# Optimization experiments

Measured on AMD Instinct MI355X. Metric: run time of the kernel, lower is better.

The kernel has to match this reference:

```python
import jax, jax.numpy as jnp
import numpy as np

B, S, D, H = 2, 2048, 2048, 16
DH = D // H            # attention_inner_dim = 128
FF = 4 * D             # feedforward_inner_dim = 8192
EPS = 1e-6


def layernorm(x, gamma, beta):
    m = jnp.mean(x, axis=-1, keepdims=True)
    v = jnp.mean((x - m) ** 2, axis=-1, keepdims=True)
    return gamma * (x - m) / jnp.sqrt(v + EPS) + beta


def rotate_half(x):
    # source rotate_half: swap halves without negation
    h = x.shape[-1] // 2
    return jnp.concatenate([x[..., h:], x[..., :h]], axis=-1)


def setup_inputs() -> dict:
    key = jax.random.key(0)
    ks = jax.random.split(key, 8)
    d = {}
    d['x'] = jax.random.normal(ks[0], (B, S, D), dtype=jnp.float32) * 0.02
    d['W_fused'] = jax.random.normal(ks[1], (D, 3 * D + FF), dtype=jnp.float32) * (D ** -0.5)
    d['b_fused'] = jnp.zeros((3 * D + FF,), dtype=jnp.float32)
    d['W_attn'] = jax.random.normal(ks[2], (D, D), dtype=jnp.float32) * (D ** -0.5)
    d['b_attn'] = jnp.zeros((D,), dtype=jnp.float32)
    d['W_ff'] = jax.random.normal(ks[3], (FF, D), dtype=jnp.float32) * (FF ** -0.5)
    d['b_ff'] = jnp.zeros((D,), dtype=jnp.float32)
    d['gamma1'] = jnp.ones((FF,), dtype=jnp.float32)
    d['beta1'] = jnp.zeros((FF,), dtype=jnp.float32)
    d['gamma2'] = jnp.ones((D,), dtype=jnp.float32)
    d['beta2'] = jnp.zeros((D,), dtype=jnp.float32)
    # learned rotary table, shape [n_positions>=S, head_dim], std = head_dim**-0.5
    d['rope_w'] = jax.random.normal(ks[4], (S, DH), dtype=jnp.float32) * (DH ** -0.5)
    return d


def reference(x, W_fused, b_fused, W_attn, b_attn, W_ff, b_ff,
              gamma1, beta1, gamma2, beta2, rope_w):
    # fused QKV + FFN projection (single GEMM)
    fused = x @ W_fused + b_fused                       # [B,S,3D+FF]
    q, k, v, ff = jnp.split(fused, [D, 2 * D, 3 * D], axis=-1)
    q = q.reshape(B, S, H, DH).transpose(0, 2, 1, 3)    # [B,H,S,DH]
    k = k.reshape(B, S, H, DH).transpose(0, 2, 1, 3)
    v = v.reshape(B, S, H, DH).transpose(0, 2, 1, 3)

    # inline rotary embedding from learned per-position table
    pe = rope_w[:S]                                     # [S,DH]
    cos, sin = jnp.cos(pe), jnp.sin(pe)

    def rope(t):
        return t * cos + rotate_half(t) * sin

    q = rope(q) * (DH ** -0.5)
    k = rope(k)

    # manual causal attention
    sim = jnp.einsum('bhqd,bhkd->bhqk', q, k)           # [B,H,S,S]
    causal = jnp.tril(jnp.ones((S, S), dtype=bool))
    sim = jnp.where(causal, sim, jnp.finfo(sim.dtype).min)
    attn_w = jax.nn.softmax(sim, axis=-1)
    o = jnp.einsum('bhqk,bhkd->bhqd', attn_w, v)        # [B,H,S,DH]
    o = o.transpose(0, 2, 1, 3).reshape(B, S, D)
    attn = o @ W_attn + b_attn                          # [B,S,D]

    # parallel feedforward branch: norm -> relu -> proj -> silu (SwiGLU in src is x*sigmoid(x))
    h = jax.nn.relu(layernorm(ff, gamma1, beta1))
    ffo = h @ W_ff + b_ff
    ffo = ffo * jax.nn.sigmoid(ffo)

    return layernorm(attn + ffo, gamma2, beta2)
```

## Files before the change

### kernel.cpp

```cpp
#include <hip/hip_runtime.h>
#include <hip/hip_bf16.h>
#include <cmath>

#define BB 2
#define SS 2048
#define DD 2048
#define HHN 16
#define DHH 128
#define FFF 8192
#define NFF (3*DD+FFF)
#define MR (BB*SS)
#define LNEPS 1e-6f

typedef __hip_bfloat16 bf16;
using bf16x8 = __attribute__((ext_vector_type(8))) __bf16;
using f32x4  = __attribute__((ext_vector_type(4))) float;

__device__ __forceinline__ void async_copy16(const bf16* g, bf16* l) {
  __builtin_amdgcn_global_load_lds(
      (const __attribute__((address_space(1))) void*)g,
      (__attribute__((address_space(3))) void*)l, 16, 0, 0);
}

__global__ __launch_bounds__(256) void k_convert(const float* __restrict__ in,
                                                 bf16* __restrict__ out, int n4) {
  int i = blockIdx.x * 256 + threadIdx.x;
  if (i >= n4) return;
  float4 v = ((const float4*)in)[i];
  out[4*i+0] = __float2bfloat16(v.x);
  out[4*i+1] = __float2bfloat16(v.y);
  out[4*i+2] = __float2bfloat16(v.z);
  out[4*i+3] = __float2bfloat16(v.w);
}

__global__ __launch_bounds__(256) void k_transpose(const float* __restrict__ in,
                                                   bf16* __restrict__ out, int R, int C) {
  __shared__ float tile[32][33];
  int c0 = blockIdx.x * 32, r0 = blockIdx.y * 32;
  int tx = threadIdx.x, ty = threadIdx.y;
  #pragma unroll
  for (int i = 0; i < 32; i += 8)
    tile[ty + i][tx] = in[(size_t)(r0 + ty + i) * C + (c0 + tx)];
  __syncthreads();
  #pragma unroll
  for (int i = 0; i < 32; i += 8)
    out[(size_t)(c0 + ty + i) * R + (r0 + tx)] = __float2bfloat16(tile[tx][ty + i]);
}

__global__ void k_vtrans(const bf16* __restrict__ fused, bf16* __restrict__ vT) {
  __shared__ bf16 tile[32][33];
  int s0 = blockIdx.x * 32, d0 = blockIdx.y * 32, bh = blockIdx.z;
  int b = bh >> 4, h = bh & 15;
  int tx = threadIdx.x, ty = threadIdx.y;
  const bf16* src = fused + (size_t)(b * SS) * NFF + 2 * DD + h * DHH;
  #pragma unroll
  for (int i = 0; i < 32; i += 8)
    tile[ty + i][tx] = src[(size_t)(s0 + ty + i) * NFF + d0 + tx];
  __syncthreads();
  bf16* dst = vT + ((size_t)bh * DHH) * SS;
  #pragma unroll
  for (int i = 0; i < 32; i += 8)
    dst[(size_t)(d0 + ty + i) * SS + s0 + tx] = tile[tx][ty + i];
}

__global__ __launch_bounds__(256) void k_gemm_bt(const bf16* __restrict__ A,
                                                 const bf16* __restrict__ BT,
                                                 const float* __restrict__ bias,
                                                 void* __restrict__ Cout,
                                                 const float* __restrict__ addin,
                                                 int M, int N, int K, int mode) {
  __shared__ __align__(16) bf16 As[128 * 32];
  __shared__ __align__(16) bf16 Bs[128 * 32];
  int NBm = M >> 7;
  constexpr int PW = 16;
  int bid = blockIdx.x;
  int pid = bid / (PW * NBm), rem = bid % (PW * NBm);
  int by = rem / PW, bx = pid * PW + rem % PW;
  int tid = threadIdx.x;
  int w = tid >> 6, l = tid & 63;
  int wm = w >> 1, wn = w & 1;
  int l15 = l & 15, g = l >> 4;
  int sr4 = l >> 2, sc4 = (l & 3) * 8;
  int m0 = by * 128, n0 = bx * 128;

  f32x4 acc[4][4];
  #pragma unroll
  for (int i = 0; i < 4; i++)
    #pragma unroll
    for (int j = 0; j < 4; j++)
      acc[i][j] = f32x4{0.f, 0.f, 0.f, 0.f};

  for (int k0 = 0; k0 < K; k0 += 32) {
    __syncthreads();
    #pragma unroll
    for (int i = 0; i < 2; i++) {
      int r = (w * 2 + i) * 16 + sr4;
      async_copy16(A + (size_t)(m0 + r) * K + k0 + sc4, &As[r * 32 + sc4]);
      async_copy16(BT + (size_t)(n0 + r) * K + k0 + sc4, &Bs[r * 32 + sc4]);
    }
    __syncthreads();

    bf16x8 af[4], bf_[4];
    #pragma unroll
    for (int i = 0; i < 4; i++)
      af[i] = *reinterpret_cast<const bf16x8*>(&As[(wm * 64 + i * 16 + l15) * 32 + g * 8]);
    #pragma unroll
    for (int j = 0; j < 4; j++)
      bf_[j] = *reinterpret_cast<const bf16x8*>(&Bs[(wn * 64 + j * 16 + l15) * 32 + g * 8]);
    #pragma unroll
    for (int i = 0; i < 4; i++)
      #pragma unroll
      for (int j = 0; j < 4; j++)
        acc[i][j] = __builtin_amdgcn_mfma_f32_16x16x32_bf16(af[i], bf_[j], acc[i][j], 0, 0, 0);
  }

  float* Cf = (float*)Cout;
  bf16* Cb = (bf16*)Cout;
  #pragma unroll
  for (int i = 0; i < 4; i++) {
    #pragma unroll
    for (int j = 0; j < 4; j++) {
      int mbase = m0 + wm * 64 + i * 16 + g * 4;
      int nn = n0 + wn * 64 + j * 16 + l15;
      float bv = bias[nn];
      #pragma unroll
      for (int rr = 0; rr < 4; rr++) {
        size_t idx = (size_t)(mbase + rr) * N + nn;
        float v = acc[i][j][rr] + bv;
        if (mode == 0) {
          Cf[idx] = v;
        } else if (mode == 1) {
          Cb[idx] = __float2bfloat16(v);
        } else {
          float sig = 1.f / (1.f + expf(-v));
          Cf[idx] = addin[idx] + v * sig;
        }
      }
    }
  }
}

__global__ __launch_bounds__(256) void k_sincos(const float* __restrict__ rope_w,
                                                float2* __restrict__ tab) {
  int i = blockIdx.x * 256 + threadIdx.x;
  if (i >= SS * DHH) return;
  float v = rope_w[i];
  tab[i] = make_float2(cosf(v), sinf(v));
}

__global__ __launch_bounds__(256) void k_rope(bf16* __restrict__ fused,
                                              const float2* __restrict__ tab) {
  int row = blockIdx.x;
  int s = row & (SS - 1);
  const float2* tr = tab + (size_t)s * DHH;
  int tid = threadIdx.x;
  int isK = tid >> 7, ch = tid & 127;
  int h = ch >> 3, c0 = (ch & 7) * 8;
  const float scale = 0.08838834764831845f;
  bf16* base = fused + (size_t)row * NFF + isK * DD + h * DHH;
  bf16x8 lo = *reinterpret_cast<const bf16x8*>(base + c0);
  bf16x8 hi = *reinterpret_cast<const bf16x8*>(base + c0 + 64);
  bf16x8 olo, ohi;
  #pragma unroll
  for (int t = 0; t < 8; t++) {
    int d = c0 + t;
    float2 cl = tr[d], chh = tr[d + 64];
    float x0 = (float)lo[t], x1 = (float)hi[t];
    float r0 = x0 * cl.x + x1 * cl.y;
    float r1 = x1 * chh.x + x0 * chh.y;
    if (!isK) { r0 *= scale; r1 *= scale; }
    olo[t] = (__bf16)r0;
    ohi[t] = (__bf16)r1;
  }
  *reinterpret_cast<bf16x8*>(base + c0) = olo;
  *reinterpret_cast<bf16x8*>(base + c0 + 64) = ohi;
}

__global__ __launch_bounds__(256) void k_flash(const bf16* __restrict__ fused,
                                               const bf16* __restrict__ vT,
                                               bf16* __restrict__ obuf) {
  __shared__ __align__(16) bf16 smem[20480];
  bf16* Ks = smem;
  bf16* Vt = smem + 8192;
  bf16* Ps = smem + 16384;
  bf16* Qs = smem;

  int qb = blockIdx.x, bh = blockIdx.y;
  int b = bh >> 4, h = bh & 15;
  int tid = threadIdx.x;
  int w = tid >> 6, l = tid & 63;
  int l15 = l & 15, g = l >> 4;

  const bf16* qbase = fused + (size_t)(b * SS + qb * 64) * NFF + h * DHH;
  const bf16* kbase = fused + (size_t)(b * SS) * NFF + DD + h * DHH;
  const bf16* vtb = vT + (size_t)bh * DHH * SS;

  #pragma unroll
  for (int ks = 0; ks < 4; ks++)
    async_copy16(qbase + (size_t)(w * 16 + (l >> 2)) * NFF + ks * 32 + (l & 3) * 8,
                 &Qs[ks * 2048 + w * 512 + l * 8]);
  __syncthreads();
  bf16x8 qf[4];
  #pragma unroll
  for (int ks = 0; ks < 4; ks++)
    qf[ks] = *reinterpret_cast<const bf16x8*>(&Qs[ks * 2048 + (w * 16 + l15) * 32 + g * 8]);

  f32x4 o[8];
  #pragma unroll
  for (int nt = 0; nt < 8; nt++) o[nt] = f32x4{0.f, 0.f, 0.f, 0.f};
  float m_i[4], l_i[4];
  #pragma unroll
  for (int r = 0; r < 4; r++) { m_i[r] = -1e30f; l_i[r] = 0.f; }
  int qrow_base = qb * 64 + w * 16 + g * 4;

  for (int kt = 0; kt <= qb; kt++) {
    __syncthreads();
    #pragma unroll
    for (int ks = 0; ks < 4; ks++)
      async_copy16(kbase + (size_t)(kt * 64 + w * 16 + (l >> 2)) * NFF + ks * 32 + (l & 3) * 8,
                   &Ks[ks * 2048 + w * 512 + l * 8]);
    #pragma unroll
    for (int j = 0; j < 2; j++)
      #pragma unroll
      for (int kc = 0; kc < 2; kc++)
        async_copy16(vtb + (size_t)(j * 64 + w * 16 + (l >> 2)) * SS + kt * 64 + kc * 32 + (l & 3) * 8,
                     &Vt[kc * 4096 + j * 2048 + w * 512 + l * 8]);
    __syncthreads();

    f32x4 s[4];
    #pragma unroll
    for (int nt = 0; nt < 4; nt++) {
      s[nt] = f32x4{0.f, 0.f, 0.f, 0.f};
      #pragma unroll
      for (int ks = 0; ks < 4; ks++) {
        bf16x8 bfrag = *reinterpret_cast<const bf16x8*>(
            &Ks[ks * 2048 + (nt * 16 + l15) * 32 + g * 8]);
        s[nt] = __builtin_amdgcn_mfma_f32_16x16x32_bf16(qf[ks], bfrag, s[nt], 0, 0, 0);
      }
    }
    #pragma unroll
    for (int nt = 0; nt < 4; nt++) {
      int kk = kt * 64 + nt * 16 + l15;
      #pragma unroll
      for (int r = 0; r < 4; r++)
        if (kk > qrow_base + r) s[nt][r] = -1e30f;
    }
    float alpha[4];
    #pragma unroll
    for (int r = 0; r < 4; r++) {
      float mx = fmaxf(fmaxf(s[0][r], s[1][r]), fmaxf(s[2][r], s[3][r]));
      mx = fmaxf(mx, __shfl_xor(mx, 1));
      mx = fmaxf(mx, __shfl_xor(mx, 2));
      mx = fmaxf(mx, __shfl_xor(mx, 4));
      mx = fmaxf(mx, __shfl_xor(mx, 8));
      float mnew = fmaxf(m_i[r], mx);
      alpha[r] = __expf(m_i[r] - mnew);
      m_i[r] = mnew;
      float ls = 0.f;
      #pragma unroll
      for (int nt = 0; nt < 4; nt++) {
        float p = __expf(s[nt][r] - mnew);
        s[nt][r] = p;
        ls += p;
      }
      ls += __shfl_xor(ls, 1);
      ls += __shfl_xor(ls, 2);
      ls += __shfl_xor(ls, 4);
      ls += __shfl_xor(ls, 8);
      l_i[r] = l_i[r] * alpha[r] + ls;
    }
    #pragma unroll
    for (int nt = 0; nt < 4; nt++) {
      int kk = nt * 16 + l15;
      #pragma unroll
      for (int r = 0; r < 4; r++)
        *(__bf16*)&Ps[(kk >> 5) * 2048 + (w * 16 + g * 4 + r) * 32 + (kk & 31)] =
            (__bf16)s[nt][r];
    }
    #pragma unroll
    for (int nt = 0; nt < 8; nt++)
      #pragma unroll
      for (int r = 0; r < 4; r++) o[nt][r] *= alpha[r];
    bf16x8 pf[2];
    #pragma unroll
    for (int ks = 0; ks < 2; ks++)
      pf[ks] = *reinterpret_cast<const bf16x8*>(
          &Ps[ks * 2048 + (w * 16 + l15) * 32 + g * 8]);
    #pragma unroll
    for (int nt = 0; nt < 8; nt++)
      #pragma unroll
      for (int ks = 0; ks < 2; ks++) {
        bf16x8 bfrag = *reinterpret_cast<const bf16x8*>(
            &Vt[ks * 4096 + (nt * 16 + l15) * 32 + g * 8]);
        o[nt] = __builtin_amdgcn_mfma_f32_16x16x32_bf16(pf[ks], bfrag, o[nt], 0, 0, 0);
      }
  }

  float inv[4];
  #pragma unroll
  for (int r = 0; r < 4; r++) inv[r] = 1.f / l_i[r];
  #pragma unroll
  for (int nt = 0; nt < 8; nt++)
    #pragma unroll
    for (int r = 0; r < 4; r++) {
      size_t row = (size_t)(b * SS + qrow_base + r);
      obuf[row * DD + h * DHH + nt * 16 + l15] = __float2bfloat16(o[nt][r] * inv[r]);
    }
}

__global__ __launch_bounds__(256) void k_ln1_relu(const bf16* __restrict__ fused,
                                                  const float* __restrict__ gamma,
                                                  const float* __restrict__ beta,
                                                  bf16* __restrict__ h) {
  int row = blockIdx.x;
  const bf16* xr = fused + (size_t)row * NFF + 3 * DD;
  int tid = threadIdx.x;
  bf16x8 v8[4];
  float s = 0.f, ss = 0.f;
  #pragma unroll
  for (int k = 0; k < 4; k++) {
    v8[k] = *reinterpret_cast<const bf16x8*>(xr + (tid + k * 256) * 8);
    #pragma unroll
    for (int t = 0; t < 8; t++) {
      float v = (float)v8[k][t];
      s += v; ss += v * v;
    }
  }
  #pragma unroll
  for (int off = 32; off > 0; off >>= 1) { s += __shfl_down(s, off); ss += __shfl_down(ss, off); }
  __shared__ float red[8];
  int wave = tid >> 6, lane = tid & 63;
  if (lane == 0) { red[wave] = s; red[4 + wave] = ss; }
  __syncthreads();
  if (tid == 0) {
    float S0 = red[0] + red[1] + red[2] + red[3];
    float SQ = red[4] + red[5] + red[6] + red[7];
    float m = S0 / FFF;
    float var = SQ / FFF - m * m;
    red[0] = m;
    red[1] = 1.f / sqrtf(var + LNEPS);
  }
  __syncthreads();
  float m = red[0], inv = red[1];
  bf16* hr = h + (size_t)row * FFF;
  #pragma unroll
  for (int k = 0; k < 4; k++) {
    bf16x8 o8;
    int base = (tid + k * 256) * 8;
    #pragma unroll
    for (int t = 0; t < 8; t++) {
      float v = (float)v8[k][t];
      float y = gamma[base + t] * (v - m) * inv + beta[base + t];
      o8[t] = (__bf16)fmaxf(y, 0.f);
    }
    *reinterpret_cast<bf16x8*>(hr + base) = o8;
  }
}

__global__ __launch_bounds__(256) void k_ln2(const float* __restrict__ yin,
                                             const float* __restrict__ gamma,
                                             const float* __restrict__ beta,
                                             float* __restrict__ out) {
  int row = blockIdx.x;
  const float4* xr = (const float4*)(yin + (size_t)row * DD);
  int tid = threadIdx.x;
  float4 v4[2];
  float s = 0.f, ss = 0.f;
  #pragma unroll
  for (int k = 0; k < 2; k++) {
    v4[k] = xr[tid + k * 256];
    s += v4[k].x + v4[k].y + v4[k].z + v4[k].w;
    ss += v4[k].x * v4[k].x + v4[k].y * v4[k].y + v4[k].z * v4[k].z + v4[k].w * v4[k].w;
  }
  #pragma unroll
  for (int off = 32; off > 0; off >>= 1) { s += __shfl_down(s, off); ss += __shfl_down(ss, off); }
  __shared__ float red[8];
  int wave = tid >> 6, lane = tid & 63;
  if (lane == 0) { red[wave] = s; red[4 + wave] = ss; }
  __syncthreads();
  if (tid == 0) {
    float S0 = red[0] + red[1] + red[2] + red[3];
    float SQ = red[4] + red[5] + red[6] + red[7];
    float m = S0 / DD;
    float var = SQ / DD - m * m;
    red[0] = m;
    red[1] = 1.f / sqrtf(var + LNEPS);
  }
  __syncthreads();
  float m = red[0], inv = red[1];
  float4* orow = (float4*)(out + (size_t)row * DD);
  #pragma unroll
  for (int k = 0; k < 2; k++) {
    int base = (tid + k * 256) * 4;
    float4 r;
    r.x = gamma[base + 0] * (v4[k].x - m) * inv + beta[base + 0];
    r.y = gamma[base + 1] * (v4[k].y - m) * inv + beta[base + 1];
    r.z = gamma[base + 2] * (v4[k].z - m) * inv + beta[base + 2];
    r.w = gamma[base + 3] * (v4[k].w - m) * inv + beta[base + 3];
    orow[tid + k * 256] = r;
  }
}

extern "C" void kernel_launch(void* const* d_in, const int* in_sizes, int n_in,
                              void* d_out, int out_size, void* d_ws, size_t ws_size,
                              hipStream_t stream) {
  const float* x       = (const float*)d_in[0];
  const float* W_fused = (const float*)d_in[1];
  const float* b_fused = (const float*)d_in[2];
  const float* W_attn  = (const float*)d_in[3];
  const float* b_attn  = (const float*)d_in[4];
  const float* W_ff    = (const float*)d_in[5];
  const float* b_ff    = (const float*)d_in[6];
  const float* gamma1  = (const float*)d_in[7];
  const float* beta1   = (const float*)d_in[8];
  const float* gamma2  = (const float*)d_in[9];
  const float* beta2   = (const float*)d_in[10];
  const float* rope_w  = (const float*)d_in[11];

  char* ws = (char*)d_ws;
  size_t off = 0;
  auto alloc = [&](size_t bytes) -> void* {
    void* p = ws + off;
    off += (bytes + 255) & ~(size_t)255;
    return p;
  };
  bf16* fused = (bf16*)alloc((size_t)MR * NFF * 2);
  bf16* xb    = (bf16*)alloc((size_t)MR * DD * 2);
  bf16* WfT   = (bf16*)alloc((size_t)NFF * DD * 2);
  bf16* WaT   = (bf16*)alloc((size_t)DD * DD * 2);
  bf16* WffT  = (bf16*)alloc((size_t)DD * FFF * 2);
  bf16* hbuf  = (bf16*)alloc((size_t)MR * FFF * 2);
  bf16* obuf  = (bf16*)alloc((size_t)MR * DD * 2);
  float* ybuf = (float*)alloc((size_t)MR * DD * 4);
  if (off > ws_size) return;
  bf16* vT = xb;
  float2* tab = (float2*)ybuf;

  k_convert<<<(MR * DD / 4 + 255) / 256, 256, 0, stream>>>(x, xb, MR * DD / 4);
  k_sincos<<<(SS * DHH + 255) / 256, 256, 0, stream>>>(rope_w, tab);
  k_transpose<<<dim3(NFF / 32, DD / 32), dim3(32, 8), 0, stream>>>(W_fused, WfT, DD, NFF);
  k_transpose<<<dim3(DD / 32, DD / 32), dim3(32, 8), 0, stream>>>(W_attn, WaT, DD, DD);
  k_transpose<<<dim3(DD / 32, FFF / 32), dim3(32, 8), 0, stream>>>(W_ff, WffT, FFF, DD);
  k_gemm_bt<<<(NFF / 128) * (MR / 128), 256, 0, stream>>>(xb, WfT, b_fused, fused, nullptr,
                                                          MR, NFF, DD, 1);
  k_rope<<<MR, 256, 0, stream>>>(fused, tab);
  k_vtrans<<<dim3(SS / 32, DHH / 32, BB * HHN), dim3(32, 8), 0, stream>>>(fused, vT);
  k_flash<<<dim3(SS / 64, BB * HHN), 256, 0, stream>>>(fused, vT, obuf);
  k_gemm_bt<<<(DD / 128) * (MR / 128), 256, 0, stream>>>(obuf, WaT, b_attn, ybuf, nullptr,
                                                         MR, DD, DD, 0);
  k_ln1_relu<<<MR, 256, 0, stream>>>(fused, gamma1, beta1, hbuf);
  k_gemm_bt<<<(DD / 128) * (MR / 128), 256, 0, stream>>>(hbuf, WffT, b_ff, ybuf, ybuf,
                                                         MR, DD, FFF, 2);
  k_ln2<<<MR, 256, 0, stream>>>(ybuf, gamma2, beta2, (float*)d_out);
}
```

Baseline: 1.176 ms.

## Switch GEMM to 32x32x16 MFMA with K=64 tiles and bf16 intermediate output

Rewrites the shared GEMM to use 32x32x16 bf16 MFMA instructions with a 64-wide K step and a k-chunk-major LDS layout, which halves the number of barrier-separated iterations and cuts LDS fragment reads per MFMA. The attention and FFN projection outputs are now stored as bf16 instead of fp32, and the final layernorm reads bf16. This reduces the intermediate buffer's memory traffic at the cost of extra rounding in the residual sum before the final norm. The rope table moves to its own buffer because ybuf is now too small to hold it.

```diff
diff --git a/kernel.cpp b/kernel.cpp
--- a/kernel.cpp
+++ b/kernel.cpp
@@ -15,6 +15,7 @@
 typedef __hip_bfloat16 bf16;
 using bf16x8 = __attribute__((ext_vector_type(8))) __bf16;
 using f32x4  = __attribute__((ext_vector_type(4))) float;
+using f32x16 = __attribute__((ext_vector_type(16))) float;
 
 __device__ __forceinline__ void async_copy16(const bf16* g, bf16* l) {
   __builtin_amdgcn_global_load_lds(
@@ -66,11 +67,11 @@
 __global__ __launch_bounds__(256) void k_gemm_bt(const bf16* __restrict__ A,
                                                  const bf16* __restrict__ BT,
                                                  const float* __restrict__ bias,
-                                                 void* __restrict__ Cout,
-                                                 const float* __restrict__ addin,
+                                                 bf16* __restrict__ Cout,
+                                                 const bf16* __restrict__ addin,
                                                  int M, int N, int K, int mode) {
-  __shared__ __align__(16) bf16 As[128 * 32];
-  __shared__ __align__(16) bf16 Bs[128 * 32];
+  __shared__ __align__(16) bf16 As[8192];
+  __shared__ __align__(16) bf16 Bs[8192];
   int NBm = M >> 7;
   constexpr int PW = 16;
   int bid = blockIdx.x;
@@ -79,62 +80,65 @@
   int tid = threadIdx.x;
   int w = tid >> 6, l = tid & 63;
   int wm = w >> 1, wn = w & 1;
-  int l15 = l & 15, g = l >> 4;
-  int sr4 = l >> 2, sc4 = (l & 3) * 8;
+  int l31 = l & 31, kg = l >> 5;
   int m0 = by * 128, n0 = bx * 128;
 
-  f32x4 acc[4][4];
-  #pragma unroll
-  for (int i = 0; i < 4; i++)
-    #pragma unroll
-    for (int j = 0; j < 4; j++)
-      acc[i][j] = f32x4{0.f, 0.f, 0.f, 0.f};
-
-  for (int k0 = 0; k0 < K; k0 += 32) {
+  f32x16 acc[2][2];
+  #pragma unroll
+  for (int i = 0; i < 2; i++)
+    #pragma unroll
+    for (int j = 0; j < 2; j++)
+      #pragma unroll
+      for (int r = 0; r < 16; r++) acc[i][j][r] = 0.f;
+
+  for (int k0 = 0; k0 < K; k0 += 64) {
     __syncthreads();
     #pragma unroll
-    for (int i = 0; i < 2; i++) {
-      int r = (w * 2 + i) * 16 + sr4;
-      async_copy16(A + (size_t)(m0 + r) * K + k0 + sc4, &As[r * 32 + sc4]);
-      async_copy16(BT + (size_t)(n0 + r) * K + k0 + sc4, &Bs[r * 32 + sc4]);
+    for (int j = 0; j < 4; j++) {
+      int i = j * 4 + w;
+      int c = i >> 1, mm = (i & 1) * 64 + l;
+      async_copy16(A + (size_t)(m0 + mm) * K + k0 + c * 8, &As[(c * 128 + mm) * 8]);
+      async_copy16(BT + (size_t)(n0 + mm) * K + k0 + c * 8, &Bs[(c * 128 + mm) * 8]);
     }
     __syncthreads();
 
-    bf16x8 af[4], bf_[4];
-    #pragma unroll
-    for (int i = 0; i < 4; i++)
-      af[i] = *reinterpret_cast<const bf16x8*>(&As[(wm * 64 + i * 16 + l15) * 32 + g * 8]);
-    #pragma unroll
-    for (int j = 0; j < 4; j++)
-      bf_[j] = *reinterpret_cast<const bf16x8*>(&Bs[(wn * 64 + j * 16 + l15) * 32 + g * 8]);
-    #pragma unroll
-    for (int i = 0; i < 4; i++)
-      #pragma unroll
-      for (int j = 0; j < 4; j++)
-        acc[i][j] = __builtin_amdgcn_mfma_f32_16x16x32_bf16(af[i], bf_[j], acc[i][j], 0, 0, 0);
-  }
-
-  float* Cf = (float*)Cout;
-  bf16* Cb = (bf16*)Cout;
-  #pragma unroll
-  for (int i = 0; i < 4; i++) {
-    #pragma unroll
-    for (int j = 0; j < 4; j++) {
-      int mbase = m0 + wm * 64 + i * 16 + g * 4;
-      int nn = n0 + wn * 64 + j * 16 + l15;
-      float bv = bias[nn];
-      #pragma unroll
-      for (int rr = 0; rr < 4; rr++) {
-        size_t idx = (size_t)(mbase + rr) * N + nn;
-        float v = acc[i][j][rr] + bv;
-        if (mode == 0) {
-          Cf[idx] = v;
-        } else if (mode == 1) {
-          Cb[idx] = __float2bfloat16(v);
-        } else {
+    #pragma unroll
+    for (int t = 0; t < 4; t++) {
+      bf16x8 af[2], bf_[2];
+      #pragma unroll
+      for (int mi = 0; mi < 2; mi++)
+        af[mi] = *reinterpret_cast<const bf16x8*>(
+            &As[((t * 2 + kg) * 128 + wm * 64 + mi * 32 + l31) * 8]);
+      #pragma unroll
+      for (int nj = 0; nj < 2; nj++)
+        bf_[nj] = *reinterpret_cast<const bf16x8*>(
+            &Bs[((t * 2 + kg) * 128 + wn * 64 + nj * 32 + l31) * 8]);
+      #pragma unroll
+      for (int mi = 0; mi < 2; mi++)
+        #pragma unroll
+        for (int nj = 0; nj < 2; nj++)
+          acc[mi][nj] = __builtin_amdgcn_mfma_f32_32x32x16_bf16(
+              af[mi], bf_[nj], acc[mi][nj], 0, 0, 0);
+    }
+  }
+
+  #pragma unroll
+  for (int mi = 0; mi < 2; mi++) {
+    #pragma unroll
+    for (int nj = 0; nj < 2; nj++) {
+      int col = n0 + wn * 64 + nj * 32 + l31;
+      int rbase = m0 + wm * 64 + mi * 32 + 4 * kg;
+      float bv = bias[col];
+      #pragma unroll
+      for (int r = 0; r < 16; r++) {
+        int row = rbase + (r & 3) + 8 * (r >> 2);
+        size_t idx = (size_t)row * N + col;
+        float v = acc[mi][nj][r] + bv;
+        if (mode == 2) {
           float sig = 1.f / (1.f + expf(-v));
-          Cf[idx] = addin[idx] + v * sig;
+          v = __bfloat162float(addin[idx]) + v * sig;
         }
+        Cout[idx] = __float2bfloat16(v);
       }
     }
   }
@@ -357,20 +361,19 @@
   }
 }
 
-__global__ __launch_bounds__(256) void k_ln2(const float* __restrict__ yin,
+__global__ __launch_bounds__(256) void k_ln2(const bf16* __restrict__ yin,
                                              const float* __restrict__ gamma,
                                              const float* __restrict__ beta,
                                              float* __restrict__ out) {
   int row = blockIdx.x;
-  const float4* xr = (const float4*)(yin + (size_t)row * DD);
+  const bf16* xr = yin + (size_t)row * DD;
   int tid = threadIdx.x;
-  float4 v4[2];
+  bf16x8 v8 = *reinterpret_cast<const bf16x8*>(xr + tid * 8);
   float s = 0.f, ss = 0.f;
   #pragma unroll
-  for (int k = 0; k < 2; k++) {
-    v4[k] = xr[tid + k * 256];
-    s += v4[k].x + v4[k].y + v4[k].z + v4[k].w;
-    ss += v4[k].x * v4[k].x + v4[k].y * v4[k].y + v4[k].z * v4[k].z + v4[k].w * v4[k].w;
+  for (int t = 0; t < 8; t++) {
+    float v = (float)v8[t];
+    s += v; ss += v * v;
   }
   #pragma unroll
   for (int off = 32; off > 0; off >>= 1) { s += __shfl_down(s, off); ss += __shfl_down(ss, off); }
@@ -391,13 +394,13 @@
   float4* orow = (float4*)(out + (size_t)row * DD);
   #pragma unroll
   for (int k = 0; k < 2; k++) {
-    int base = (tid + k * 256) * 4;
+    int base = tid * 8 + k * 4;
     float4 r;
-    r.x = gamma[base + 0] * (v4[k].x - m) * inv + beta[base + 0];
-    r.y = gamma[base + 1] * (v4[k].y - m) * inv + beta[base + 1];
-    r.z = gamma[base + 2] * (v4[k].z - m) * inv + beta[base + 2];
-    r.w = gamma[base + 3] * (v4[k].w - m) * inv + beta[base + 3];
-    orow[tid + k * 256] = r;
+    r.x = gamma[base + 0] * ((float)v8[k * 4 + 0] - m) * inv + beta[base + 0];
+    r.y = gamma[base + 1] * ((float)v8[k * 4 + 1] - m) * inv + beta[base + 1];
+    r.z = gamma[base + 2] * ((float)v8[k * 4 + 2] - m) * inv + beta[base + 2];
+    r.w = gamma[base + 3] * ((float)v8[k * 4 + 3] - m) * inv + beta[base + 3];
+    orow[tid * 2 + k] = r;
   }
 }
 
@@ -431,10 +434,11 @@
   bf16* WffT  = (bf16*)alloc((size_t)DD * FFF * 2);
   bf16* hbuf  = (bf16*)alloc((size_t)MR * FFF * 2);
   bf16* obuf  = (bf16*)alloc((size_t)MR * DD * 2);
-  float* ybuf = (float*)alloc((size_t)MR * DD * 4);
+  bf16* ybuf  = (bf16*)alloc((size_t)MR * DD * 2);
+  float* tabf = (float*)alloc((size_t)SS * DHH * 8);
   if (off > ws_size) return;
   bf16* vT = xb;
-  float2* tab = (float2*)ybuf;
+  float2* tab = (float2*)tabf;
 
   k_convert<<<(MR * DD / 4 + 255) / 256, 256, 0, stream>>>(x, xb, MR * DD / 4);
   k_sincos<<<(SS * DHH + 255) / 256, 256, 0, stream>>>(rope_w, tab);
```

Result: slower. 1.511 ms (+28.4%).

## Enlarge flash query tile to 128 rows and store attention/FFN output in bf16

Applied to the files above, without the earlier changes.

The flash attention kernel now gives each block 128 query rows, with each wave handling two 16-row sub-tiles. Every K/V tile loaded into LDS is therefore reused for twice as many queries, which halves K/V global traffic and the number of blocks. Separately, the intermediate attention-plus-FFN sum ybuf is kept in bf16 instead of fp32, which cuts its memory traffic and changes the precision of the final layernorm input. The rope table gets its own workspace buffer, and waves skip fully masked tiles; fewer blocks may reduce occupancy and load balance on the causal triangle.

```diff
diff --git a/kernel.cpp b/kernel.cpp
--- a/kernel.cpp
+++ b/kernel.cpp
@@ -66,8 +66,8 @@
 __global__ __launch_bounds__(256) void k_gemm_bt(const bf16* __restrict__ A,
                                                  const bf16* __restrict__ BT,
                                                  const float* __restrict__ bias,
-                                                 void* __restrict__ Cout,
-                                                 const float* __restrict__ addin,
+                                                 bf16* __restrict__ Cout,
+                                                 const bf16* __restrict__ addin,
                                                  int M, int N, int K, int mode) {
   __shared__ __align__(16) bf16 As[128 * 32];
   __shared__ __align__(16) bf16 Bs[128 * 32];
@@ -114,8 +114,6 @@
         acc[i][j] = __builtin_amdgcn_mfma_f32_16x16x32_bf16(af[i], bf_[j], acc[i][j], 0, 0, 0);
   }
 
-  float* Cf = (float*)Cout;
-  bf16* Cb = (bf16*)Cout;
   #pragma unroll
   for (int i = 0; i < 4; i++) {
     #pragma unroll
@@ -127,14 +125,11 @@
       for (int rr = 0; rr < 4; rr++) {
         size_t idx = (size_t)(mbase + rr) * N + nn;
         float v = acc[i][j][rr] + bv;
-        if (mode == 0) {
-          Cf[idx] = v;
-        } else if (mode == 1) {
-          Cb[idx] = __float2bfloat16(v);
-        } else {
+        if (mode == 2) {
           float sig = 1.f / (1.f + expf(-v));
-          Cf[idx] = addin[idx] + v * sig;
+          v = __bfloat162float(addin[idx]) + v * sig;
         }
+        Cout[idx] = __float2bfloat16(v);
       }
     }
   }
@@ -179,7 +174,7 @@
 __global__ __launch_bounds__(256) void k_flash(const bf16* __restrict__ fused,
                                                const bf16* __restrict__ vT,
                                                bf16* __restrict__ obuf) {
-  __shared__ __align__(16) bf16 smem[20480];
+  __shared__ __align__(16) bf16 smem[24576];
   bf16* Ks = smem;
   bf16* Vt = smem + 8192;
   bf16* Ps = smem + 16384;
@@ -191,29 +186,41 @@
   int w = tid >> 6, l = tid & 63;
   int l15 = l & 15, g = l >> 4;
 
-  const bf16* qbase = fused + (size_t)(b * SS + qb * 64) * NFF + h * DHH;
+  const bf16* qbase = fused + (size_t)(b * SS + qb * 128) * NFF + h * DHH;
   const bf16* kbase = fused + (size_t)(b * SS) * NFF + DD + h * DHH;
   const bf16* vtb = vT + (size_t)bh * DHH * SS;
 
   #pragma unroll
   for (int ks = 0; ks < 4; ks++)
-    async_copy16(qbase + (size_t)(w * 16 + (l >> 2)) * NFF + ks * 32 + (l & 3) * 8,
-                 &Qs[ks * 2048 + w * 512 + l * 8]);
-  __syncthreads();
-  bf16x8 qf[4];
-  #pragma unroll
-  for (int ks = 0; ks < 4; ks++)
-    qf[ks] = *reinterpret_cast<const bf16x8*>(&Qs[ks * 2048 + (w * 16 + l15) * 32 + g * 8]);
-
-  f32x4 o[8];
-  #pragma unroll
-  for (int nt = 0; nt < 8; nt++) o[nt] = f32x4{0.f, 0.f, 0.f, 0.f};
-  float m_i[4], l_i[4];
-  #pragma unroll
-  for (int r = 0; r < 4; r++) { m_i[r] = -1e30f; l_i[r] = 0.f; }
-  int qrow_base = qb * 64 + w * 16 + g * 4;
-
-  for (int kt = 0; kt <= qb; kt++) {
+    #pragma unroll
+    for (int j = 0; j < 2; j++) {
+      int row = w * 32 + j * 16 + (l >> 2);
+      async_copy16(qbase + (size_t)row * NFF + ks * 32 + (l & 3) * 8,
+                   &Qs[ks * 4096 + row * 32 + (l & 3) * 8]);
+    }
+  __syncthreads();
+  bf16x8 qf[2][4];
+  #pragma unroll
+  for (int p = 0; p < 2; p++)
+    #pragma unroll
+    for (int ks = 0; ks < 4; ks++)
+      qf[p][ks] = *reinterpret_cast<const bf16x8*>(
+          &Qs[ks * 4096 + (w * 32 + p * 16 + l15) * 32 + g * 8]);
+
+  f32x4 o[2][8];
+  #pragma unroll
+  for (int p = 0; p < 2; p++)
+    #pragma unroll
+    for (int nt = 0; nt < 8; nt++) o[p][nt] = f32x4{0.f, 0.f, 0.f, 0.f};
+  float m_i[2][4], l_i[2][4];
+  #pragma unroll
+  for (int p = 0; p < 2; p++)
+    #pragma unroll
+    for (int r = 0; r < 4; r++) { m_i[p][r] = -1e30f; l_i[p][r] = 0.f; }
+  int qrow0 = qb * 128 + w * 32 + g * 4;
+
+  int ntiles = 2 * qb + 2;
+  for (int kt = 0; kt < ntiles; kt++) {
     __syncthreads();
     #pragma unroll
     for (int ks = 0; ks < 4; ks++)
@@ -227,85 +234,98 @@
                      &Vt[kc * 4096 + j * 2048 + w * 512 + l * 8]);
     __syncthreads();
 
-    f32x4 s[4];
+    if (kt * 64 > qb * 128 + w * 32 + 31) continue;
+
+    f32x4 s[2][4];
     #pragma unroll
     for (int nt = 0; nt < 4; nt++) {
-      s[nt] = f32x4{0.f, 0.f, 0.f, 0.f};
+      s[0][nt] = f32x4{0.f, 0.f, 0.f, 0.f};
+      s[1][nt] = f32x4{0.f, 0.f, 0.f, 0.f};
       #pragma unroll
       for (int ks = 0; ks < 4; ks++) {
         bf16x8 bfrag = *reinterpret_cast<const bf16x8*>(
             &Ks[ks * 2048 + (nt * 16 + l15) * 32 + g * 8]);
-        s[nt] = __builtin_amdgcn_mfma_f32_16x16x32_bf16(qf[ks], bfrag, s[nt], 0, 0, 0);
-      }
-    }
-    #pragma unroll
-    for (int nt = 0; nt < 4; nt++) {
-      int kk = kt * 64 + nt * 16 + l15;
-      #pragma unroll
-      for (int r = 0; r < 4; r++)
-        if (kk > qrow_base + r) s[nt][r] = -1e30f;
-    }
-    float alpha[4];
-    #pragma unroll
-    for (int r = 0; r < 4; r++) {
-      float mx = fmaxf(fmaxf(s[0][r], s[1][r]), fmaxf(s[2][r], s[3][r]));
-      mx = fmaxf(mx, __shfl_xor(mx, 1));
-      mx = fmaxf(mx, __shfl_xor(mx, 2));
-      mx = fmaxf(mx, __shfl_xor(mx, 4));
-      mx = fmaxf(mx, __shfl_xor(mx, 8));
-      float mnew = fmaxf(m_i[r], mx);
-      alpha[r] = __expf(m_i[r] - mnew);
-      m_i[r] = mnew;
-      float ls = 0.f;
+        s[0][nt] = __builtin_amdgcn_mfma_f32_16x16x32_bf16(qf[0][ks], bfrag, s[0][nt], 0, 0, 0);
+        s[1][nt] = __builtin_amdgcn_mfma_f32_16x16x32_bf16(qf[1][ks], bfrag, s[1][nt], 0, 0, 0);
+      }
+    }
+    float alpha[2][4];
+    #pragma unroll
+    for (int p = 0; p < 2; p++) {
       #pragma unroll
       for (int nt = 0; nt < 4; nt++) {
-        float p = __expf(s[nt][r] - mnew);
-        s[nt][r] = p;
-        ls += p;
-      }
-      ls += __shfl_xor(ls, 1);
-      ls += __shfl_xor(ls, 2);
-      ls += __shfl_xor(ls, 4);
-      ls += __shfl_xor(ls, 8);
-      l_i[r] = l_i[r] * alpha[r] + ls;
-    }
-    #pragma unroll
-    for (int nt = 0; nt < 4; nt++) {
-      int kk = nt * 16 + l15;
-      #pragma unroll
-      for (int r = 0; r < 4; r++)
-        *(__bf16*)&Ps[(kk >> 5) * 2048 + (w * 16 + g * 4 + r) * 32 + (kk & 31)] =
-            (__bf16)s[nt][r];
-    }
+        int kk = kt * 64 + nt * 16 + l15;
+        #pragma unroll
+        for (int r = 0; r < 4; r++)
+          if (kk > qrow0 + p * 16 + r) s[p][nt][r] = -1e30f;
+      }
+      #pragma unroll
+      for (int r = 0; r < 4; r++) {
+        float mx = fmaxf(fmaxf(s[p][0][r], s[p][1][r]), fmaxf(s[p][2][r], s[p][3][r]));
+        mx = fmaxf(mx, __shfl_xor(mx, 1));
+        mx = fmaxf(mx, __shfl_xor(mx, 2));
+        mx = fmaxf(mx, __shfl_xor(mx, 4));
+        mx = fmaxf(mx, __shfl_xor(mx, 8));
+        float mnew = fmaxf(m_i[p][r], mx);
+        alpha[p][r] = __expf(m_i[p][r] - mnew);
+        m_i[p][r] = mnew;
+        float ls = 0.f;
+        #pragma unroll
+        for (int nt = 0; nt < 4; nt++) {
+          float pv = __expf(s[p][nt][r] - mnew);
+          s[p][nt][r] = pv;
+          ls += pv;
+        }
+        ls += __shfl_xor(ls, 1);
+        ls += __shfl_xor(ls, 2);
+        ls += __shfl_xor(ls, 4);
+        ls += __shfl_xor(ls, 8);
+        l_i[p][r] = l_i[p][r] * alpha[p][r] + ls;
+      }
+      #pragma unroll
+      for (int nt = 0; nt < 4; nt++) {
+        int kk = nt * 16 + l15;
+        #pragma unroll
+        for (int r = 0; r < 4; r++)
+          *(__bf16*)&Ps[(kk >> 5) * 4096 + (w * 32 + p * 16 + g * 4 + r) * 32 + (kk & 31)] =
+              (__bf16)s[p][nt][r];
+      }
+      #pragma unroll
+      for (int nt = 0; nt < 8; nt++)
+        #pragma unroll
+        for (int r = 0; r < 4; r++) o[p][nt][r] *= alpha[p][r];
+    }
+    bf16x8 pf[2][2];
+    #pragma unroll
+    for (int p = 0; p < 2; p++)
+      #pragma unroll
+      for (int kc = 0; kc < 2; kc++)
+        pf[p][kc] = *reinterpret_cast<const bf16x8*>(
+            &Ps[kc * 4096 + (w * 32 + p * 16 + l15) * 32 + g * 8]);
     #pragma unroll
     for (int nt = 0; nt < 8; nt++)
       #pragma unroll
-      for (int r = 0; r < 4; r++) o[nt][r] *= alpha[r];
-    bf16x8 pf[2];
-    #pragma unroll
-    for (int ks = 0; ks < 2; ks++)
-      pf[ks] = *reinterpret_cast<const bf16x8*>(
-          &Ps[ks * 2048 + (w * 16 + l15) * 32 + g * 8]);
+      for (int kc = 0; kc < 2; kc++) {
+        bf16x8 bfrag = *reinterpret_cast<const bf16x8*>(
+            &Vt[kc * 4096 + (nt * 16 + l15) * 32 + g * 8]);
+        o[0][nt] = __builtin_amdgcn_mfma_f32_16x16x32_bf16(pf[0][kc], bfrag, o[0][nt], 0, 0, 0);
+        o[1][nt] = __builtin_amdgcn_mfma_f32_16x16x32_bf16(pf[1][kc], bfrag, o[1][nt], 0, 0, 0);
+      }
+  }
+
+  #pragma unroll
+  for (int p = 0; p < 2; p++) {
+    float inv[4];
+    #pragma unroll
+    for (int r = 0; r < 4; r++) inv[r] = 1.f / l_i[p][r];
     #pragma unroll
     for (int nt = 0; nt < 8; nt++)
       #pragma unroll
-      for (int ks = 0; ks < 2; ks++) {
-        bf16x8 bfrag = *reinterpret_cast<const bf16x8*>(
-            &Vt[ks * 4096 + (nt * 16 + l15) * 32 + g * 8]);
-        o[nt] = __builtin_amdgcn_mfma_f32_16x16x32_bf16(pf[ks], bfrag, o[nt], 0, 0, 0);
-      }
-  }
-
-  float inv[4];
-  #pragma unroll
-  for (int r = 0; r < 4; r++) inv[r] = 1.f / l_i[r];
-  #pragma unroll
-  for (int nt = 0; nt < 8; nt++)
-    #pragma unroll
-    for (int r = 0; r < 4; r++) {
-      size_t row = (size_t)(b * SS + qrow_base + r);
-      obuf[row * DD + h * DHH + nt * 16 + l15] = __float2bfloat16(o[nt][r] * inv[r]);
-    }
+      for (int r = 0; r < 4; r++) {
+        size_t row = (size_t)(b * SS + qrow0 + p * 16 + r);
+        obuf[row * DD + h * DHH + nt * 16 + l15] = __float2bfloat16(o[p][nt][r] * inv[r]);
+      }
+  }
 }
 
 __global__ __launch_bounds__(256) void k_ln1_relu(const bf16* __restrict__ fused,
@@ -357,20 +377,19 @@
   }
 }
 
-__global__ __launch_bounds__(256) void k_ln2(const float* __restrict__ yin,
+__global__ __launch_bounds__(256) void k_ln2(const bf16* __restrict__ yin,
                                              const float* __restrict__ gamma,
                                              const float* __restrict__ beta,
                                              float* __restrict__ out) {
   int row = blockIdx.x;
-  const float4* xr = (const float4*)(yin + (size_t)row * DD);
+  const bf16* xr = yin + (size_t)row * DD;
   int tid = threadIdx.x;
-  float4 v4[2];
+  bf16x8 v8 = *reinterpret_cast<const bf16x8*>(xr + tid * 8);
   float s = 0.f, ss = 0.f;
   #pragma unroll
-  for (int k = 0; k < 2; k++) {
-    v4[k] = xr[tid + k * 256];
-    s += v4[k].x + v4[k].y + v4[k].z + v4[k].w;
-    ss += v4[k].x * v4[k].x + v4[k].y * v4[k].y + v4[k].z * v4[k].z + v4[k].w * v4[k].w;
+  for (int t = 0; t < 8; t++) {
+    float v = (float)v8[t];
+    s += v; ss += v * v;
   }
   #pragma unroll
   for (int off = 32; off > 0; off >>= 1) { s += __shfl_down(s, off); ss += __shfl_down(ss, off); }
@@ -391,13 +410,13 @@
   float4* orow = (float4*)(out + (size_t)row * DD);
   #pragma unroll
   for (int k = 0; k < 2; k++) {
-    int base = (tid + k * 256) * 4;
+    int base = tid * 8 + k * 4;
     float4 r;
-    r.x = gamma[base + 0] * (v4[k].x - m) * inv + beta[base + 0];
-    r.y = gamma[base + 1] * (v4[k].y - m) * inv + beta[base + 1];
-    r.z = gamma[base + 2] * (v4[k].z - m) * inv + beta[base + 2];
-    r.w = gamma[base + 3] * (v4[k].w - m) * inv + beta[base + 3];
-    orow[tid + k * 256] = r;
+    r.x = gamma[base + 0] * ((float)v8[k * 4 + 0] - m) * inv + beta[base + 0];
+    r.y = gamma[base + 1] * ((float)v8[k * 4 + 1] - m) * inv + beta[base + 1];
+    r.z = gamma[base + 2] * ((float)v8[k * 4 + 2] - m) * inv + beta[base + 2];
+    r.w = gamma[base + 3] * ((float)v8[k * 4 + 3] - m) * inv + beta[base + 3];
+    orow[tid * 2 + k] = r;
   }
 }
 
@@ -431,10 +450,11 @@
   bf16* WffT  = (bf16*)alloc((size_t)DD * FFF * 2);
   bf16* hbuf  = (bf16*)alloc((size_t)MR * FFF * 2);
   bf16* obuf  = (bf16*)alloc((size_t)MR * DD * 2);
-  float* ybuf = (float*)alloc((size_t)MR * DD * 4);
+  bf16* ybuf  = (bf16*)alloc((size_t)MR * DD * 2);
+  float* tabf = (float*)alloc((size_t)SS * DHH * 8);
   if (off > ws_size) return;
   bf16* vT = xb;
-  float2* tab = (float2*)ybuf;
+  float2* tab = (float2*)tabf;
 
   k_convert<<<(MR * DD / 4 + 255) / 256, 256, 0, stream>>>(x, xb, MR * DD / 4);
   k_sincos<<<(SS * DHH + 255) / 256, 256, 0, stream>>>(rope_w, tab);
@@ -445,7 +465,7 @@
                                                           MR, NFF, DD, 1);
   k_rope<<<MR, 256, 0, stream>>>(fused, tab);
   k_vtrans<<<dim3(SS / 32, DHH / 32, BB * HHN), dim3(32, 8), 0, stream>>>(fused, vT);
-  k_flash<<<dim3(SS / 64, BB * HHN), 256, 0, stream>>>(fused, vT, obuf);
+  k_flash<<<dim3(SS / 128, BB * HHN), 256, 0, stream>>>(fused, vT, obuf);
   k_gemm_bt<<<(DD / 128) * (MR / 128), 256, 0, stream>>>(obuf, WaT, b_attn, ybuf, nullptr,
                                                          MR, DD, DD, 0);
   k_ln1_relu<<<MR, 256, 0, stream>>>(fused, gamma1, beta1, hbuf);
```

After: 1.135 ms. -3.5%, faster.
